# Kernel tuning notes

Measured on AMD Instinct MI355X. Metric: run time of the kernel, lower is better.

Reference implementation:

```python
import jax, jax.numpy as jnp
import numpy as np

B, S, H, NH, NE = 4, 1024, 256, 4, 4
D = H // NH  # head_unit = 64
EPS = 1e-8


def layernorm(x, g, b):
    m = jnp.mean(x, axis=-1, keepdims=True)
    v = jnp.mean((x - m) ** 2, axis=-1, keepdims=True)
    return (x - m) / jnp.sqrt(v + EPS) * g + b


def setup_inputs() -> dict:
    key = jax.random.key(0)
    ks = jax.random.split(key, 18)
    sc = 0.05
    return {
        "x": jax.random.normal(ks[0], (B, S, H), jnp.float32),
        # MoEMultiHead params
        "hl_w": jax.random.normal(ks[1], (NH, D, H), jnp.float32) * sc,   # head_layer weights (out,in)
        "hl_b": jax.random.normal(ks[2], (NH, D), jnp.float32) * sc,
        "wq": jax.random.normal(ks[3], (NH, NE, D, D), jnp.float32) * sc,  # w_q[i*NH+j] -> wq[i,j]
        "wk": jax.random.normal(ks[4], (NH, D, D), jnp.float32) * sc,
        "wv": jax.random.normal(ks[5], (NH, D, D), jnp.float32) * sc,
        "gate_w": jax.random.normal(ks[6], (NH, NE, NE * D), jnp.float32) * sc,
        "gate_b": jax.random.normal(ks[7], (NH, NE), jnp.float32) * sc,
        "ln_g": jnp.ones((D,), jnp.float32),
        "ln_b": jnp.zeros((D,), jnp.float32),
        # FFN params (built inside forward in torch; materialized here)
        "fc1_w": jax.random.normal(ks[8], (D, D), jnp.float32) * sc,
        "fc1_b": jax.random.normal(ks[9], (D,), jnp.float32) * sc,
        "fc2_w": jax.random.normal(ks[10], (D, D), jnp.float32) * sc,
        "fc2_b": jax.random.normal(ks[11], (D,), jnp.float32) * sc,
        "fnorm_g": jnp.ones((D,), jnp.float32),
        "fnorm_b": jnp.zeros((D,), jnp.float32),
        "fgate_w": jax.random.normal(ks[12], (NH, H), jnp.float32) * sc,
    }


def reference(x, hl_w, hl_b, wq, wk, wv, gate_w, gate_b, ln_g, ln_b,
              fc1_w, fc1_b, fc2_w, fc2_b, fnorm_g, fnorm_b, fgate_w):
    b, s, h = x.shape
    nh, d, _ = wk.shape
    ne = wq.shape[1]
    # per-head projection of full hidden -> head_unit  (B, NH, S, D)
    sx = jnp.einsum('bsh,ndh->bnsd', x, hl_w) + hl_b[None, :, None, :]
    pad = sx == 0  # padding mask, same for all experts
    # per-(head, expert) q; per-head k, v
    q = jnp.einsum('bnsd,neod->bneso', sx, wq)       # (B,NH,NE,S,D)
    k = jnp.einsum('bnsd,nod->bnso', sx, wk)         # (B,NH,S,D)
    v = jnp.einsum('bnsd,nod->bnso', sx, wv)
    causal = jnp.where(jnp.tril(jnp.ones((s, s), bool)), 0.0, -jnp.inf).astype(x.dtype)
    # NOTE: original MULTIPLIES by sqrt(head_unit) (bug-faithful)
    scores = jnp.einsum('bnesd,bntd->bnest', q, k) * (d ** 0.5) + causal
    att = jax.nn.softmax(scores, axis=-1)
    qkv = jnp.einsum('bnest,bntd->bnesd', att, v)
    qkv = jnp.where(pad[:, :, None], 0.0, qkv)
    # concat experts along feature dim: (B,NH,S,NE*D)
    out = jnp.transpose(qkv, (0, 1, 3, 2, 4)).reshape(b, nh, s, ne * d)
    gs = jax.nn.softmax(jnp.einsum('bnsf,nef->bnse', out, gate_w) + gate_b[None, :, None, :], axis=-1)
    mixed = jnp.einsum('bnsed,bnse->bnsd', out.reshape(b, nh, s, ne, d), gs)
    # bug-faithful residual: split_x[i] indexes the BATCH dim with head index i
    resid = sx[jnp.arange(nh), jnp.arange(nh)]  # (NH, S, D), broadcast over batch
    hn = layernorm(mixed + resid, ln_g, ln_b)   # (B,NH,S,D); dropout inactive (p=0)
    f_n = jnp.transpose(hn, (0, 2, 1, 3)).reshape(b, s, h)
    # ---- FFN (fresh module in torch; deterministic params here) ----
    fx = f_n.reshape(b, s, nh, d)  # torch.split along feature dim
    pm = fx == 0
    hx = jnp.where(pm, 0.0, fx @ fc1_w.T + fc1_b)
    hx = jax.nn.relu(hx)
    hx = jnp.where(pm, 0.0, hx @ fc2_w.T + fc2_b)
    hx = layernorm(hx + fx, fnorm_g, fnorm_b)
    fout = hx.reshape(b, s, h)
    fg = jax.nn.softmax(fout @ fgate_w.T, axis=-1)  # (B,S,NH)
    return (fout.reshape(b, s, nh, d) * fg[..., None]).reshape(b, s, h)
```

## Files before the change

kernel.cpp:

```cpp
#include <hip/hip_runtime.h>
#include <math.h>

typedef unsigned short u16;
typedef __attribute__((ext_vector_type(8))) unsigned short us8;
typedef __attribute__((ext_vector_type(4))) unsigned short us4;
typedef __attribute__((ext_vector_type(8))) short bf16x8;
typedef __attribute__((ext_vector_type(4))) float f32x4;

constexpr int B_ = 4, S_ = 1024, H_ = 256, NH_ = 4, NE_ = 4, D_ = 64;
constexpr float EPS_ = 1e-8f;

__device__ __forceinline__ u16 f2bf(float f){
  unsigned u = __float_as_uint(f);
  unsigned rnd = 0x7fffu + ((u>>16)&1u);
  return (u16)((u + rnd)>>16);
}
__device__ __forceinline__ us8 pack8(float4 a, float4 b){
  us8 r;
  r[0]=f2bf(a.x); r[1]=f2bf(a.y); r[2]=f2bf(a.z); r[3]=f2bf(a.w);
  r[4]=f2bf(b.x); r[5]=f2bf(b.y); r[6]=f2bf(b.z); r[7]=f2bf(b.w);
  return r;
}
#define MFMA16(a,b,c) __builtin_amdgcn_mfma_f32_16x16x32_bf16((bf16x8)(a),(bf16x8)(b),(c),0,0,0)

__global__ __launch_bounds__(256) void k_sx(const float* __restrict__ x, const float* __restrict__ hlw,
                                            const float* __restrict__ hlb,
                                            float* __restrict__ sx, u16* __restrict__ sxb){
  int mt = blockIdx.x >> 3, nt = blockIdx.x & 7;
  int tid = threadIdx.x, w = tid>>6, l = tid&63, lr = l>>4, lc = l&15;
  __shared__ u16 Xs[64*64];
  __shared__ u16 Ws[32*64];
  const int swl = (lc&7)<<3;
  f32x4 acc[2] = {{0,0,0,0},{0,0,0,0}};
  for(int ks=0; ks<4; ++ks){
    __syncthreads();
    #pragma unroll
    for(int it=0; it<2; ++it){
      int c0 = w*8 + it*32;
      const float* xp = x + ((size_t)(mt*64+l))*H_ + ks*64 + c0;
      float4 a = *(const float4*)xp, b = *(const float4*)(xp+4);
      *(us8*)&Xs[l*64 + (c0 ^ ((l&7)<<3))] = pack8(a,b);
    }
    { int row = tid&31, c0 = (tid>>5)*8;
      const float* wp = hlw + ((size_t)(nt*32+row))*H_ + ks*64 + c0;
      float4 a = *(const float4*)wp, b = *(const float4*)(wp+4);
      *(us8*)&Ws[row*64 + (c0 ^ ((row&7)<<3))] = pack8(a,b);
    }
    __syncthreads();
    bf16x8 a0 = *(const bf16x8*)&Xs[(w*16+lc)*64 + ((lr*8   ) ^ swl)];
    bf16x8 a1 = *(const bf16x8*)&Xs[(w*16+lc)*64 + ((lr*8+32) ^ swl)];
    #pragma unroll
    for(int j=0;j<2;j++){
      const u16* wr = &Ws[(j*16+lc)*64];
      bf16x8 b0 = *(const bf16x8*)(wr + ((lr*8   ) ^ swl));
      bf16x8 b1 = *(const bf16x8*)(wr + ((lr*8+32) ^ swl));
      acc[j] = MFMA16(a0,b0,acc[j]);
      acc[j] = MFMA16(a1,b1,acc[j]);
    }
  }
  #pragma unroll
  for(int j=0;j<2;j++){
    int col = nt*32 + j*16 + lc;
    int n = col>>6, d = col&63;
    float bias = hlb[col];
    #pragma unroll
    for(int r=0;r<4;r++){
      int m = mt*64 + w*16 + lr*4 + r;
      int b = m>>10, s = m&1023;
      float v = acc[j][r] + bias;
      size_t idx = ((size_t)(b*NH_+n)*S_+s)*D_ + d;
      sx[idx] = v; sxb[idx] = f2bf(v);
    }
  }
}

__global__ __launch_bounds__(256) void k_qkv(const u16* __restrict__ sxb, const float* __restrict__ wq,
            const float* __restrict__ wk, const float* __restrict__ wv,
            u16* __restrict__ qb, u16* __restrict__ kbf, u16* __restrict__ vbf){
  int bid = blockIdx.x;
  int half = bid&1, mt = (bid>>1)&63, n = bid>>7;
  int tid = threadIdx.x, w = tid>>6, l = tid&63, lr = l>>4, lc = l&15;
  __shared__ u16 As[64*64];
  __shared__ u16 Ws[192*64];
  const int swl = (lc&7)<<3;
  int b = (mt*64)>>10, s0 = (mt*64)&1023;
  #pragma unroll
  for(int it=0; it<2; ++it){
    int c0 = w*8 + it*32;
    us8 v = *(const us8*)(sxb + ((size_t)(b*NH_+n)*S_ + s0 + l)*D_ + c0);
    *(us8*)&As[l*64 + (c0 ^ ((l&7)<<3))] = v;
  }
  #pragma unroll
  for(int ch=0; ch<3; ++ch){
    int o = half*192 + ch*64 + l;
    const float* src;
    if(o < 256)      src = wq + ((size_t)((n*NE_ + (o>>6))*D_ + (o&63)))*D_;
    else if(o < 320) src = wk + ((size_t)(n*D_ + (o-256)))*D_;
    else             src = wv + ((size_t)(n*D_ + (o-320)))*D_;
    #pragma unroll
    for(int it=0; it<2; ++it){
      int c0 = w*8 + it*32;
      float4 a = *(const float4*)(src+c0), bb = *(const float4*)(src+c0+4);
      *(us8*)&Ws[(ch*64+l)*64 + (c0 ^ ((l&7)<<3))] = pack8(a,bb);
    }
  }
  __syncthreads();
  bf16x8 a0 = *(const bf16x8*)&As[(w*16+lc)*64 + ((lr*8   ) ^ swl)];
  bf16x8 a1 = *(const bf16x8*)&As[(w*16+lc)*64 + ((lr*8+32) ^ swl)];
  f32x4 acc[12];
  #pragma unroll
  for(int j=0;j<12;j++) acc[j] = (f32x4){0,0,0,0};
  #pragma unroll
  for(int j=0;j<12;j++){
    const u16* wr = &Ws[(j*16+lc)*64];
    bf16x8 b0 = *(const bf16x8*)(wr + ((lr*8   ) ^ swl));
    bf16x8 b1 = *(const bf16x8*)(wr + ((lr*8+32) ^ swl));
    acc[j] = MFMA16(a0,b0,acc[j]);
    acc[j] = MFMA16(a1,b1,acc[j]);
  }
  #pragma unroll
  for(int j=0;j<12;j++){
    int o = half*192 + j*16 + lc;
    #pragma unroll
    for(int r=0;r<4;r++){
      int s = s0 + w*16 + lr*4 + r;
      float v = acc[j][r];
      if(o < 256){
        int e = o>>6, d = o&63;
        qb[((size_t)((b*NH_+n)*NE_+e)*S_ + s)*D_ + d] = f2bf(v*11.5415603f);
      } else if(o < 320){
        kbf[((size_t)(b*NH_+n)*S_ + s)*D_ + (o-256)] = f2bf(v);
      } else {
        vbf[((size_t)(b*NH_+n)*S_ + s)*D_ + (o-320)] = f2bf(v);
      }
    }
  }
}

__global__ __launch_bounds__(256,4) void k_attn(const u16* __restrict__ qb, const u16* __restrict__ kb,
        const u16* __restrict__ vb, const float* __restrict__ sx, float* __restrict__ attout){
  int bid = blockIdx.x;
  int head = bid & 63, idx = bid >> 6;
  int g = idx>>2, pos = idx&3;
  int qt = (g&1) ? (15 - (g>>1) - 2*pos) : ((g>>1) + 2*pos);
  int bq = head>>2, e = head&3;
  int tid = threadIdx.x, w = tid>>6, l = tid&63, lr = l>>4, lc = l&15;
  __shared__ u16 Ks[2][64*64];
  __shared__ u16 VT[2][64*64];
  __shared__ u16 Pb[4][16*64];
  const u16* kh = kb + (size_t)bq*S_*D_;
  const u16* vh = vb + (size_t)bq*S_*D_;
  const int swl = (lc&7)<<3;
  const int swst = (l&7)<<3;

  const u16* qrow = qb + ((size_t)head*S_ + qt*64 + w*16 + lc)*D_;
  bf16x8 qf0 = *(const bf16x8*)(qrow + lr*8);
  bf16x8 qf1 = *(const bf16x8*)(qrow + lr*8 + 32);
  f32x4 Oa[4];
  #pragma unroll
  for(int j=0;j<4;j++) Oa[j] = (f32x4){0,0,0,0};
  float m_i = -INFINITY, l_i = 0.f;

  us8 rg[4];
  {
    const u16* kr = kh + (size_t)l*D_;
    const u16* vr = vh + (size_t)l*D_;
    int c0 = w*8;
    rg[0] = *(const us8*)(kr + c0);      rg[1] = *(const us8*)(kr + c0 + 32);
    rg[2] = *(const us8*)(vr + c0);      rg[3] = *(const us8*)(vr + c0 + 32);
    *(us8*)&Ks[0][l*64 + ( c0      ^ swst)] = rg[0];
    *(us8*)&Ks[0][l*64 + ((c0+32)  ^ swst)] = rg[1];
    #pragma unroll
    for(int i=0;i<8;i++){ int d=c0+i;    VT[0][d*64 + (l ^ ((d&7)<<3))] = rg[2][i]; }
    #pragma unroll
    for(int i=0;i<8;i++){ int d=c0+32+i; VT[0][d*64 + (l ^ ((d&7)<<3))] = rg[3][i]; }
  }
  for(int kt=0; kt<=qt; ++kt){
    int cur = kt&1;
    __syncthreads();
    bool more = kt < qt;
    if(more){
      const u16* kr = kh + ((size_t)(kt+1)*64 + l)*D_;
      const u16* vr = vh + ((size_t)(kt+1)*64 + l)*D_;
      int c0 = w*8;
      rg[0] = *(const us8*)(kr + c0);    rg[1] = *(const us8*)(kr + c0 + 32);
      rg[2] = *(const us8*)(vr + c0);    rg[3] = *(const us8*)(vr + c0 + 32);
    }
    f32x4 Sa[4];
    #pragma unroll
    for(int j=0;j<4;j++){
      const u16* kr = &Ks[cur][(j*16+lc)*64];
      bf16x8 a0 = *(const bf16x8*)(kr + ((lr*8   ) ^ swl));
      bf16x8 a1 = *(const bf16x8*)(kr + ((lr*8+32) ^ swl));
      f32x4 z = (f32x4){0,0,0,0};
      z = MFMA16(a0,qf0,z);
      z = MFMA16(a1,qf1,z);
      Sa[j] = z;
    }
    if(kt==qt){
      int q = w*16 + lc;
      #pragma unroll
      for(int j=0;j<4;j++)
        #pragma unroll
        for(int r=0;r<4;r++)
          if(j*16 + lr*4 + r > q) Sa[j][r] = -INFINITY;
    }
    float mx0 = fmaxf(fmaxf(Sa[0][0],Sa[0][1]),fmaxf(Sa[0][2],Sa[0][3]));
    float mx1 = fmaxf(fmaxf(Sa[1][0],Sa[1][1]),fmaxf(Sa[1][2],Sa[1][3]));
    float mx2 = fmaxf(fmaxf(Sa[2][0],Sa[2][1]),fmaxf(Sa[2][2],Sa[2][3]));
    float mx3 = fmaxf(fmaxf(Sa[3][0],Sa[3][1]),fmaxf(Sa[3][2],Sa[3][3]));
    float mx = fmaxf(fmaxf(mx0,mx1),fmaxf(mx2,mx3));
    mx = fmaxf(mx, __shfl_xor(mx,16));
    mx = fmaxf(mx, __shfl_xor(mx,32));
    float mn = fmaxf(m_i, mx);
    float scale = exp2f(m_i - mn);
    #pragma unroll
    for(int j=0;j<4;j++)
      #pragma unroll
      for(int r=0;r<4;r++) Sa[j][r] = exp2f(Sa[j][r] - mn);
    float rs0 = (Sa[0][0]+Sa[0][1]) + (Sa[0][2]+Sa[0][3]);
    float rs1 = (Sa[1][0]+Sa[1][1]) + (Sa[1][2]+Sa[1][3]);
    float rs2 = (Sa[2][0]+Sa[2][1]) + (Sa[2][2]+Sa[2][3]);
    float rs3 = (Sa[3][0]+Sa[3][1]) + (Sa[3][2]+Sa[3][3]);
    float rs = (rs0+rs1) + (rs2+rs3);
    rs += __shfl_xor(rs,16);
    rs += __shfl_xor(rs,32);
    l_i = l_i*scale + rs;
    m_i = mn;
    #pragma unroll
    for(int jd=0;jd<4;jd++)
      #pragma unroll
      for(int r=0;r<4;r++) Oa[jd][r] *= scale;
    #pragma unroll
    for(int j=0;j<4;j++){
      us4 pk;
      #pragma unroll
      for(int r=0;r<4;r++) pk[r] = f2bf(Sa[j][r]);
      *(us4*)&Pb[w][lc*64 + ((j*16+lr*4) ^ swl)] = pk;
    }
    asm volatile("s_waitcnt lgkmcnt(0)" ::: "memory");
    bf16x8 pB0 = *(const bf16x8*)&Pb[w][lc*64 + ((lr*8   ) ^ swl)];
    bf16x8 pB1 = *(const bf16x8*)&Pb[w][lc*64 + ((lr*8+32) ^ swl)];
    #pragma unroll
    for(int jd=0;jd<4;jd++){
      const u16* vr = &VT[cur][(jd*16+lc)*64];
      bf16x8 v0 = *(const bf16x8*)(vr + ((lr*8   ) ^ swl));
      bf16x8 v1 = *(const bf16x8*)(vr + ((lr*8+32) ^ swl));
      Oa[jd] = MFMA16(v0,pB0,Oa[jd]);
      Oa[jd] = MFMA16(v1,pB1,Oa[jd]);
    }
    if(more){
      int nb = cur^1, c0 = w*8;
      *(us8*)&Ks[nb][l*64 + ( c0     ^ swst)] = rg[0];
      *(us8*)&Ks[nb][l*64 + ((c0+32) ^ swst)] = rg[1];
      #pragma unroll
      for(int i=0;i<8;i++){ int d=c0+i;    VT[nb][d*64 + (l ^ ((d&7)<<3))] = rg[2][i]; }
      #pragma unroll
      for(int i=0;i<8;i++){ int d=c0+32+i; VT[nb][d*64 + (l ^ ((d&7)<<3))] = rg[3][i]; }
    }
  }
  int qg = qt*64 + w*16 + lc;
  float inv = 1.f/l_i;
  const float* sxp = sx + ((size_t)bq*S_ + qg)*D_;
  float* op = attout + ((size_t)bq*S_ + qg)*(NE_*D_) + e*D_;
  #pragma unroll
  for(int jd=0;jd<4;jd++){
    int d0 = jd*16 + lr*4;
    f32x4 sxv = *(const f32x4*)(sxp + d0);
    f32x4 ov;
    #pragma unroll
    for(int r=0;r<4;r++){
      float o = Oa[jd][r]*inv;
      ov[r] = (sxv[r]==0.f) ? 0.f : o;
    }
    *(f32x4*)(op + d0) = ov;
  }
}

__global__ __launch_bounds__(256) void k_tail(const float* __restrict__ attout, const float* __restrict__ gw,
      const float* __restrict__ gb, const float* __restrict__ sx,
      const float* __restrict__ lng, const float* __restrict__ lnb,
      const float* __restrict__ w1g, const float* __restrict__ b1g,
      const float* __restrict__ w2g, const float* __restrict__ b2g,
      const float* __restrict__ fng, const float* __restrict__ fnb,
      const float* __restrict__ fgw, float* __restrict__ out){
  int bid = blockIdx.x;
  int gs0 = bid*16, b = gs0>>10, s0 = gs0&1023;
  int tid = threadIdx.x;
  int row = tid>>4, l16 = tid&15;
  int w = tid>>6, l = tid&63, lr = l>>4, lc = l&15;
  __shared__ float Fx[64][64];
  __shared__ u16 FnB[64*64];
  __shared__ u16 W1[64*64], W2[64*64], H1[64*64];
  __shared__ float Red[4][16][4];

  #pragma unroll
  for(int g2=0; g2<2; ++g2){
    int g = tid*2+g2; int r2 = g>>3, c0 = (g&7)*8;
    float4 a = *(const float4*)(w1g + r2*64 + c0), bb = *(const float4*)(w1g + r2*64 + c0 + 4);
    *(us8*)&W1[r2*64 + (c0 ^ ((r2&7)<<3))] = pack8(a,bb);
    a = *(const float4*)(w2g + r2*64 + c0); bb = *(const float4*)(w2g + r2*64 + c0 + 4);
    *(us8*)&W2[r2*64 + (c0 ^ ((r2&7)<<3))] = pack8(a,bb);
  }
  const int d0 = l16*4;
  for(int n=0;n<NH_;++n){
    f32x4 o[4];
    const float* ar = attout + ((size_t)(b*NH_+n)*S_ + s0 + row)*(NE_*D_);
    #pragma unroll
    for(int e=0;e<4;e++) o[e] = *(const f32x4*)(ar + e*64 + d0);
    float lg4[4];
    #pragma unroll
    for(int eg=0; eg<4; ++eg){
      const float* gr = gw + (size_t)(n*NE_+eg)*(NE_*D_);
      float p = 0.f;
      #pragma unroll
      for(int e=0;e<4;e++){
        f32x4 g4 = *(const f32x4*)(gr + e*64 + d0);
        p += o[e][0]*g4[0] + o[e][1]*g4[1] + o[e][2]*g4[2] + o[e][3]*g4[3];
      }
      #pragma unroll
      for(int off=1; off<16; off<<=1) p += __shfl_xor(p, off);
      lg4[eg] = p + gb[n*NE_+eg];
    }
    float mx = fmaxf(fmaxf(lg4[0],lg4[1]),fmaxf(lg4[2],lg4[3]));
    float se = 0.f;
    #pragma unroll
    for(int eg=0;eg<4;eg++){ lg4[eg]=__expf(lg4[eg]-mx); se+=lg4[eg]; }
    float inv = 1.f/se;
    f32x4 res = *(const f32x4*)(sx + ((size_t)(n*NH_+n)*S_ + s0 + row)*D_ + d0);
    float tv[4];
    #pragma unroll
    for(int k=0;k<4;k++){
      float mixk = o[0][k]*lg4[0] + o[1][k]*lg4[1] + o[2][k]*lg4[2] + o[3][k]*lg4[3];
      tv[k] = mixk*inv + res[k];
    }
    float sum = tv[0]+tv[1]+tv[2]+tv[3];
    #pragma unroll
    for(int off=1; off<16; off<<=1) sum += __shfl_xor(sum, off);
    float mean = sum*(1.f/64.f);
    float vs = 0.f;
    #pragma unroll
    for(int k=0;k<4;k++){ float d = tv[k]-mean; vs += d*d; }
    #pragma unroll
    for(int off=1; off<16; off<<=1) vs += __shfl_xor(vs, off);
    float rstd = rsqrtf(vs*(1.f/64.f)+EPS_);
    f32x4 lgv = *(const f32x4*)(lng + d0);
    f32x4 lbv = *(const f32x4*)(lnb + d0);
    int hr = n*16+row;
    us4 pk;
    f32x4 yv;
    #pragma unroll
    for(int k=0;k<4;k++){
      float y = (tv[k]-mean)*rstd*lgv[k] + lbv[k];
      yv[k] = y; pk[k] = f2bf(y);
    }
    *(f32x4*)&Fx[hr][d0] = yv;
    *(us4*)&FnB[hr*64 + (d0 ^ ((hr&7)<<3))] = pk;
  }
  __syncthreads();
  const int swl = (lc&7)<<3;
  bf16x8 a0 = *(const bf16x8*)&FnB[(w*16+lc)*64 + ((lr*8   ) ^ swl)];
  bf16x8 a1 = *(const bf16x8*)&FnB[(w*16+lc)*64 + ((lr*8+32) ^ swl)];
  f32x4 acc1[4];
  #pragma unroll
  for(int jn=0;jn<4;jn++) acc1[jn] = (f32x4){0,0,0,0};
  #pragma unroll
  for(int jn=0;jn<4;jn++){
    const u16* wr = &W1[(jn*16+lc)*64];
    bf16x8 b0 = *(const bf16x8*)(wr + ((lr*8   ) ^ swl));
    bf16x8 b1 = *(const bf16x8*)(wr + ((lr*8+32) ^ swl));
    acc1[jn] = MFMA16(a0,b0,acc1[jn]);
    acc1[jn] = MFMA16(a1,b1,acc1[jn]);
  }
  #pragma unroll
  for(int jn=0;jn<4;jn++){
    int dout = jn*16+lc;
    float bias = b1g[dout];
    #pragma unroll
    for(int rr=0;rr<4;rr++){
      int hr = w*16 + lr*4 + rr;
      float v = acc1[jn][rr] + bias;
      v = (Fx[hr][dout]==0.f) ? 0.f : v;
      v = fmaxf(v, 0.f);
      H1[hr*64 + (dout ^ ((hr&7)<<3))] = f2bf(v);
    }
  }
  __syncthreads();
  a0 = *(const bf16x8*)&H1[(w*16+lc)*64 + ((lr*8   ) ^ swl)];
  a1 = *(const bf16x8*)&H1[(w*16+lc)*64 + ((lr*8+32) ^ swl)];
  f32x4 acc2[4];
  #pragma unroll
  for(int jn=0;jn<4;jn++) acc2[jn] = (f32x4){0,0,0,0};
  #pragma unroll
  for(int jn=0;jn<4;jn++){
    const u16* wr = &W2[(jn*16+lc)*64];
    bf16x8 b0 = *(const bf16x8*)(wr + ((lr*8   ) ^ swl));
    bf16x8 b1 = *(const bf16x8*)(wr + ((lr*8+32) ^ swl));
    acc2[jn] = MFMA16(a0,b0,acc2[jn]);
    acc2[jn] = MFMA16(a1,b1,acc2[jn]);
  }
  float tv2[4][4];
  #pragma unroll
  for(int jn=0;jn<4;jn++){
    int dout = jn*16+lc;
    float bias = b2g[dout];
    #pragma unroll
    for(int rr=0;rr<4;rr++){
      int hr = w*16 + lr*4 + rr;
      float fx = Fx[hr][dout];
      float v = acc2[jn][rr] + bias;
      v = (fx==0.f) ? 0.f : v;
      tv2[jn][rr] = v + fx;
    }
  }
  float sum_r[4], vs_r[4];
  #pragma unroll
  for(int rr=0;rr<4;rr++) sum_r[rr] = tv2[0][rr]+tv2[1][rr]+tv2[2][rr]+tv2[3][rr];
  #pragma unroll
  for(int off=1; off<16; off<<=1)
    #pragma unroll
    for(int rr=0;rr<4;rr++) sum_r[rr] += __shfl_xor(sum_r[rr], off);
  float mean_r[4];
  #pragma unroll
  for(int rr=0;rr<4;rr++) mean_r[rr] = sum_r[rr]*(1.f/64.f);
  #pragma unroll
  for(int rr=0;rr<4;rr++){
    float a = tv2[0][rr]-mean_r[rr], b2v = tv2[1][rr]-mean_r[rr];
    float c = tv2[2][rr]-mean_r[rr], d = tv2[3][rr]-mean_r[rr];
    vs_r[rr] = a*a + b2v*b2v + c*c + d*d;
  }
  #pragma unroll
  for(int off=1; off<16; off<<=1)
    #pragma unroll
    for(int rr=0;rr<4;rr++) vs_r[rr] += __shfl_xor(vs_r[rr], off);
  float y2[4][4];
  #pragma unroll
  for(int jn=0;jn<4;jn++){
    int dout = jn*16+lc;
    float g = fng[dout], bb = fnb[dout];
    #pragma unroll
    for(int rr=0;rr<4;rr++){
      float rstd = rsqrtf(vs_r[rr]*(1.f/64.f)+EPS_);
      y2[jn][rr] = (tv2[jn][rr]-mean_r[rr])*rstd*g + bb;
    }
  }
  float fg4[4][4];
  #pragma unroll
  for(int j=0;j<4;j++)
    #pragma unroll
    for(int jn=0;jn<4;jn++)
      fg4[j][jn] = fgw[(size_t)j*H_ + w*64 + jn*16 + lc];
  float pj[4][4];
  #pragma unroll
  for(int j=0;j<4;j++)
    #pragma unroll
    for(int rr=0;rr<4;rr++)
      pj[j][rr] = y2[0][rr]*fg4[j][0] + y2[1][rr]*fg4[j][1] + y2[2][rr]*fg4[j][2] + y2[3][rr]*fg4[j][3];
  #pragma unroll
  for(int off=1; off<16; off<<=1)
    #pragma unroll
    for(int j=0;j<4;j++)
      #pragma unroll
      for(int rr=0;rr<4;rr++) pj[j][rr] += __shfl_xor(pj[j][rr], off);
  if(lc==0){
    #pragma unroll
    for(int rr=0;rr<4;rr++)
      #pragma unroll
      for(int j=0;j<4;j++) Red[w][lr*4+rr][j] = pj[j][rr];
  }
  __syncthreads();
  #pragma unroll
  for(int rr=0;rr<4;rr++){
    int srow = lr*4+rr;
    float lgf[4];
    #pragma unroll
    for(int j=0;j<4;j++) lgf[j] = Red[0][srow][j]+Red[1][srow][j]+Red[2][srow][j]+Red[3][srow][j];
    float mx2 = fmaxf(fmaxf(lgf[0],lgf[1]),fmaxf(lgf[2],lgf[3]));
    float se2 = 0.f;
    #pragma unroll
    for(int j=0;j<4;j++){ lgf[j]=__expf(lgf[j]-mx2); se2+=lgf[j]; }
    float gsn = lgf[w]/se2;
    float* op = out + ((size_t)(gs0 + srow))*H_ + w*64;
    #pragma unroll
    for(int jn=0;jn<4;jn++) op[jn*16+lc] = y2[jn][rr]*gsn;
  }
}

extern "C" void kernel_launch(void* const* d_in, const int* in_sizes, int n_in,
                              void* d_out, int out_size, void* d_ws, size_t ws_size,
                              hipStream_t stream){
  const float* x      = (const float*)d_in[0];
  const float* hl_w   = (const float*)d_in[1];
  const float* hl_b   = (const float*)d_in[2];
  const float* wq     = (const float*)d_in[3];
  const float* wk     = (const float*)d_in[4];
  const float* wv     = (const float*)d_in[5];
  const float* gate_w = (const float*)d_in[6];
  const float* gate_b = (const float*)d_in[7];
  const float* ln_g   = (const float*)d_in[8];
  const float* ln_b   = (const float*)d_in[9];
  const float* fc1_w  = (const float*)d_in[10];
  const float* fc1_b  = (const float*)d_in[11];
  const float* fc2_w  = (const float*)d_in[12];
  const float* fc2_b  = (const float*)d_in[13];
  const float* fnorm_g= (const float*)d_in[14];
  const float* fnorm_b= (const float*)d_in[15];
  const float* fgate_w= (const float*)d_in[16];

  const size_t NSD = (size_t)B_*NH_*S_*D_;
  float* ws     = (float*)d_ws;
  float* sx     = ws;
  float* attout = sx + NSD;
  float* f_n    = attout + NSD*NE_;
  u16*   sxb    = (u16*)(f_n + NSD);
  u16*   qb     = sxb + NSD;
  u16*   kbf    = qb + NSD*NE_;
  u16*   vbf    = kbf + NSD;

  k_sx  <<<512,  256, 0, stream>>>(x, hl_w, hl_b, sx, sxb);
  k_qkv <<<512,  256, 0, stream>>>(sxb, wq, wk, wv, qb, kbf, vbf);
  k_attn<<<1024, 256, 0, stream>>>(qb, kbf, vbf, sx, attout);
  k_tail<<<256,  256, 0, stream>>>(attout, gate_w, gate_b, sx, ln_g, ln_b,
                                   fc1_w, fc1_b, fc2_w, fc2_b,
                                   fnorm_g, fnorm_b, fgate_w, (float*)d_out);
}
```

Baseline: 67.06 us.

## Store V transposed from QKV kernel and pass attention output as bf16

The QKV kernel now writes V in a transposed (D,S) layout, so the attention kernel can fill its V^T shared tile with vectorized 16-byte stores instead of scalar transposing stores. The attention output and the padding-mask source (sx) are also read and written as bf16 rather than fp32, which halves the intermediate traffic between the attention and tail kernels. The transposed V write in k_qkv is strided and scattered, and the lower precision of the attention output may change numerics slightly. The padding test now checks bf16 zero, which differs from the fp32 check only for tiny values.

```diff
diff --git a/kernel.cpp b/kernel.cpp
--- a/kernel.cpp
+++ b/kernel.cpp
@@ -15,6 +15,7 @@
   unsigned rnd = 0x7fffu + ((u>>16)&1u);
   return (u16)((u + rnd)>>16);
 }
+__device__ __forceinline__ float bf2f(u16 u){ return __uint_as_float(((unsigned)u)<<16); }
 __device__ __forceinline__ us8 pack8(float4 a, float4 b){
   us8 r;
   r[0]=f2bf(a.x); r[1]=f2bf(a.y); r[2]=f2bf(a.z); r[3]=f2bf(a.w);
@@ -76,7 +77,7 @@
 
 __global__ __launch_bounds__(256) void k_qkv(const u16* __restrict__ sxb, const float* __restrict__ wq,
             const float* __restrict__ wk, const float* __restrict__ wv,
-            u16* __restrict__ qb, u16* __restrict__ kbf, u16* __restrict__ vbf){
+            u16* __restrict__ qb, u16* __restrict__ kbf, u16* __restrict__ vbT){
   int bid = blockIdx.x;
   int half = bid&1, mt = (bid>>1)&63, n = bid>>7;
   int tid = threadIdx.x, w = tid>>6, l = tid&63, lr = l>>4, lc = l&15;
@@ -131,14 +132,15 @@
       } else if(o < 320){
         kbf[((size_t)(b*NH_+n)*S_ + s)*D_ + (o-256)] = f2bf(v);
       } else {
-        vbf[((size_t)(b*NH_+n)*S_ + s)*D_ + (o-320)] = f2bf(v);
+        int d = o-320;
+        vbT[((size_t)(b*NH_+n)*D_ + d)*S_ + s] = f2bf(v);
       }
     }
   }
 }
 
 __global__ __launch_bounds__(256,4) void k_attn(const u16* __restrict__ qb, const u16* __restrict__ kb,
-        const u16* __restrict__ vb, const float* __restrict__ sx, float* __restrict__ attout){
+        const u16* __restrict__ vbT, const u16* __restrict__ sxb, u16* __restrict__ attoutb){
   int bid = blockIdx.x;
   int head = bid & 63, idx = bid >> 6;
   int g = idx>>2, pos = idx&3;
@@ -148,8 +150,8 @@
   __shared__ u16 Ks[2][64*64];
   __shared__ u16 VT[2][64*64];
   __shared__ u16 Pb[4][16*64];
-  const u16* kh = kb + (size_t)bq*S_*D_;
-  const u16* vh = vb + (size_t)bq*S_*D_;
+  const u16* kh = kb  + (size_t)bq*S_*D_;
+  const u16* vh = vbT + (size_t)bq*D_*S_;
   const int swl = (lc&7)<<3;
   const int swst = (l&7)<<3;
 
@@ -163,28 +165,26 @@
 
   us8 rg[4];
   {
-    const u16* kr = kh + (size_t)l*D_;
-    const u16* vr = vh + (size_t)l*D_;
     int c0 = w*8;
-    rg[0] = *(const us8*)(kr + c0);      rg[1] = *(const us8*)(kr + c0 + 32);
-    rg[2] = *(const us8*)(vr + c0);      rg[3] = *(const us8*)(vr + c0 + 32);
-    *(us8*)&Ks[0][l*64 + ( c0      ^ swst)] = rg[0];
-    *(us8*)&Ks[0][l*64 + ((c0+32)  ^ swst)] = rg[1];
-    #pragma unroll
-    for(int i=0;i<8;i++){ int d=c0+i;    VT[0][d*64 + (l ^ ((d&7)<<3))] = rg[2][i]; }
-    #pragma unroll
-    for(int i=0;i<8;i++){ int d=c0+32+i; VT[0][d*64 + (l ^ ((d&7)<<3))] = rg[3][i]; }
+    rg[0] = *(const us8*)(kh + (size_t)l*D_ + c0);
+    rg[1] = *(const us8*)(kh + (size_t)l*D_ + c0 + 32);
+    rg[2] = *(const us8*)(vh + (size_t)l*S_ + c0);
+    rg[3] = *(const us8*)(vh + (size_t)l*S_ + c0 + 32);
+    *(us8*)&Ks[0][l*64 + ( c0     ^ swst)] = rg[0];
+    *(us8*)&Ks[0][l*64 + ((c0+32) ^ swst)] = rg[1];
+    *(us8*)&VT[0][l*64 + ( c0     ^ swst)] = rg[2];
+    *(us8*)&VT[0][l*64 + ((c0+32) ^ swst)] = rg[3];
   }
   for(int kt=0; kt<=qt; ++kt){
     int cur = kt&1;
     __syncthreads();
     bool more = kt < qt;
     if(more){
-      const u16* kr = kh + ((size_t)(kt+1)*64 + l)*D_;
-      const u16* vr = vh + ((size_t)(kt+1)*64 + l)*D_;
       int c0 = w*8;
-      rg[0] = *(const us8*)(kr + c0);    rg[1] = *(const us8*)(kr + c0 + 32);
-      rg[2] = *(const us8*)(vr + c0);    rg[3] = *(const us8*)(vr + c0 + 32);
+      rg[0] = *(const us8*)(kh + ((size_t)(kt+1)*64 + l)*D_ + c0);
+      rg[1] = *(const us8*)(kh + ((size_t)(kt+1)*64 + l)*D_ + c0 + 32);
+      rg[2] = *(const us8*)(vh + (size_t)l*S_ + (kt+1)*64 + c0);
+      rg[3] = *(const us8*)(vh + (size_t)l*S_ + (kt+1)*64 + c0 + 32);
     }
     f32x4 Sa[4];
     #pragma unroll
@@ -253,31 +253,29 @@
       int nb = cur^1, c0 = w*8;
       *(us8*)&Ks[nb][l*64 + ( c0     ^ swst)] = rg[0];
       *(us8*)&Ks[nb][l*64 + ((c0+32) ^ swst)] = rg[1];
-      #pragma unroll
-      for(int i=0;i<8;i++){ int d=c0+i;    VT[nb][d*64 + (l ^ ((d&7)<<3))] = rg[2][i]; }
-      #pragma unroll
-      for(int i=0;i<8;i++){ int d=c0+32+i; VT[nb][d*64 + (l ^ ((d&7)<<3))] = rg[3][i]; }
+      *(us8*)&VT[nb][l*64 + ( c0     ^ swst)] = rg[2];
+      *(us8*)&VT[nb][l*64 + ((c0+32) ^ swst)] = rg[3];
     }
   }
   int qg = qt*64 + w*16 + lc;
   float inv = 1.f/l_i;
-  const float* sxp = sx + ((size_t)bq*S_ + qg)*D_;
-  float* op = attout + ((size_t)bq*S_ + qg)*(NE_*D_) + e*D_;
+  const u16* sxp = sxb + ((size_t)bq*S_ + qg)*D_;
+  u16* op = attoutb + ((size_t)bq*S_ + qg)*(NE_*D_) + e*D_;
   #pragma unroll
   for(int jd=0;jd<4;jd++){
     int d0 = jd*16 + lr*4;
-    f32x4 sxv = *(const f32x4*)(sxp + d0);
-    f32x4 ov;
+    us4 sxv = *(const us4*)(sxp + d0);
+    us4 ov;
     #pragma unroll
     for(int r=0;r<4;r++){
       float o = Oa[jd][r]*inv;
-      ov[r] = (sxv[r]==0.f) ? 0.f : o;
-    }
-    *(f32x4*)(op + d0) = ov;
-  }
-}
-
-__global__ __launch_bounds__(256) void k_tail(const float* __restrict__ attout, const float* __restrict__ gw,
+      ov[r] = ((sxv[r]&0x7fff)==0) ? (u16)0 : f2bf(o);
+    }
+    *(us4*)(op + d0) = ov;
+  }
+}
+
+__global__ __launch_bounds__(256) void k_tail(const u16* __restrict__ attoutb, const float* __restrict__ gw,
       const float* __restrict__ gb, const float* __restrict__ sx,
       const float* __restrict__ lng, const float* __restrict__ lnb,
       const float* __restrict__ w1g, const float* __restrict__ b1g,
@@ -305,9 +303,13 @@
   const int d0 = l16*4;
   for(int n=0;n<NH_;++n){
     f32x4 o[4];
-    const float* ar = attout + ((size_t)(b*NH_+n)*S_ + s0 + row)*(NE_*D_);
-    #pragma unroll
-    for(int e=0;e<4;e++) o[e] = *(const f32x4*)(ar + e*64 + d0);
+    const u16* ar = attoutb + ((size_t)(b*NH_+n)*S_ + s0 + row)*(NE_*D_);
+    #pragma unroll
+    for(int e=0;e<4;e++){
+      us4 t = *(const us4*)(ar + e*64 + d0);
+      #pragma unroll
+      for(int k=0;k<4;k++) o[e][k] = bf2f(t[k]);
+    }
     float lg4[4];
     #pragma unroll
     for(int eg=0; eg<4; ++eg){
@@ -508,19 +510,18 @@
   const float* fgate_w= (const float*)d_in[16];
 
   const size_t NSD = (size_t)B_*NH_*S_*D_;
-  float* ws     = (float*)d_ws;
-  float* sx     = ws;
-  float* attout = sx + NSD;
-  float* f_n    = attout + NSD*NE_;
-  u16*   sxb    = (u16*)(f_n + NSD);
-  u16*   qb     = sxb + NSD;
-  u16*   kbf    = qb + NSD*NE_;
-  u16*   vbf    = kbf + NSD;
+  float* ws      = (float*)d_ws;
+  float* sx      = ws;
+  u16*   sxb     = (u16*)(sx + NSD);
+  u16*   attoutb = sxb + NSD;
+  u16*   qb      = attoutb + NSD*NE_;
+  u16*   kbf     = qb + NSD*NE_;
+  u16*   vbT     = kbf + NSD;
 
   k_sx  <<<512,  256, 0, stream>>>(x, hl_w, hl_b, sx, sxb);
-  k_qkv <<<512,  256, 0, stream>>>(sxb, wq, wk, wv, qb, kbf, vbf);
-  k_attn<<<1024, 256, 0, stream>>>(qb, kbf, vbf, sx, attout);
-  k_tail<<<256,  256, 0, stream>>>(attout, gate_w, gate_b, sx, ln_g, ln_b,
+  k_qkv <<<512,  256, 0, stream>>>(sxb, wq, wk, wv, qb, kbf, vbT);
+  k_attn<<<1024, 256, 0, stream>>>(qb, kbf, vbT, sxb, attoutb);
+  k_tail<<<256,  256, 0, stream>>>(attoutb, gate_w, gate_b, sx, ln_g, ln_b,
                                    fc1_w, fc1_b, fc2_w, fc2_b,
                                    fnorm_g, fnorm_b, fgate_w, (float*)d_out);
 }
```

Measured after the change: 67.74 us. Within noise of the previous version (+1.0%).
